# Optimization experiments

Measured on AMD Instinct MI355X. Metric: run time of the kernel, lower is better.

## Reference

```python
import jax, jax.numpy as jnp
import numpy as np
from jax import lax

S, B, C = 128, 32, 16
VW, VC = 100000, 100
DW, DC = 256, 64
HW, HC = 512, 128
T = 17


def setup_inputs():
    key = jax.random.key(0)
    it = iter(jax.random.split(key, 40))

    def p(shape, scale=0.05):
        return jax.random.normal(next(it), shape, jnp.float32) * scale

    inp = {}
    inp['sentence'] = jax.random.randint(next(it), (S, B), 2, VW)
    inp['char'] = jax.random.randint(next(it), (B, S, C), 2, VC)
    inp['tags'] = jax.random.randint(next(it), (S, B), 0, T)
    inp['W_we'] = p((VW, DW)).at[1].set(0.0)  # padding_idx=1 row zeroed
    inp['W_ce'] = p((VC, DC)).at[1].set(0.0)
    Hc2, Hw2 = HC // 2, HW // 2
    for d in ('f', 'b'):
        inp['c_Wih_' + d] = p((4 * Hc2, DC))
        inp['c_Whh_' + d] = p((4 * Hc2, Hc2))
        inp['c_b_' + d] = p((4 * Hc2,))
        inp['w_Wih_' + d] = p((4 * Hw2, DW + HC))
        inp['w_Whh_' + d] = p((4 * Hw2, Hw2))
        inp['w_b_' + d] = p((4 * Hw2,))
    inp['emit_W'] = p((T, HW))
    inp['emit_b'] = p((T,))
    inp['crf_trans'] = p((T, T), 0.1)
    inp['crf_start'] = p((T,), 0.1)
    inp['crf_end'] = p((T,), 0.1)
    return inp


def _lstm(xs, Wih, Whh, b):
    # xs: (L, N, D); torch gate order i,f,g,o
    H = Whh.shape[1]

    def step(carry, x):
        h, c = carry
        g = x @ Wih.T + h @ Whh.T + b
        i, f, gg, o = jnp.split(g, 4, axis=-1)
        c = jax.nn.sigmoid(f) * c + jax.nn.sigmoid(i) * jnp.tanh(gg)
        h = jax.nn.sigmoid(o) * jnp.tanh(c)
        return (h, c), h

    z = jnp.zeros((xs.shape[1], H), xs.dtype)
    (hT, _), hs = lax.scan(step, (z, z), xs)
    return hs, hT


def _bilstm(xs, Wf, Uf, bf, Wb, Ub, bb):
    hs_f, hT_f = _lstm(xs, Wf, Uf, bf)
    hs_b, hT_b = _lstm(xs[::-1], Wb, Ub, bb)
    return jnp.concatenate([hs_f, hs_b[::-1]], axis=-1), hT_f, hT_b


def _crf_nll(em, tags, mask, trans, start, end):
    # em: (S,B,T); pytorch-crf log-likelihood, reduction='sum'; returns -llh
    b_idx = jnp.arange(em.shape[1])
    mf = mask.astype(em.dtype)
    score0 = start[tags[0]] + em[0, b_idx, tags[0]]

    def num_step(carry, inp):
        s, prev = carry
        e_t, t_t, m_t = inp
        s = s + (trans[prev, t_t] + e_t[b_idx, t_t]) * m_t
        prev = jnp.where(m_t > 0, t_t, prev)
        return (s, prev), None

    (num, last), _ = lax.scan(num_step, (score0, tags[0]), (em[1:], tags[1:], mf[1:]))
    num = num + end[last]

    alpha0 = start[None, :] + em[0]

    def den_step(alpha, inp):
        e_t, m_t = inp
        nxt = jax.scipy.special.logsumexp(alpha[:, :, None] + trans[None] + e_t[:, None, :], axis=1)
        return jnp.where(m_t[:, None] > 0, nxt, alpha), None

    alpha, _ = lax.scan(den_step, alpha0, (em[1:], mf[1:]))
    den = jax.scipy.special.logsumexp(alpha + end[None, :], axis=1)
    return -jnp.sum(num - den)


def reference(sentence, char, tags, W_we, W_ce, c_Wih_f, c_Whh_f, c_b_f, c_Wih_b, c_Whh_b, c_b_b, w_Wih_f, w_Whh_f, w_b_f, w_Wih_b, w_Whh_b, w_b_b, emit_W, emit_b, crf_trans, crf_start, crf_end):
    # char features: batch the per-position char BiLSTM across (B*S)
    ce = W_ce[char]  # (B,S,C,DC)
    ce = jnp.transpose(ce, (2, 0, 1, 3)).reshape(C, B * S, DC)
    _, hTf, hTb = _bilstm(ce, c_Wih_f, c_Whh_f, c_b_f, c_Wih_b, c_Whh_b, c_b_b)
    ch = jnp.concatenate([hTf, hTb], axis=-1).reshape(B, S, HC).transpose(1, 0, 2)  # (S,B,HC)
    x = jnp.concatenate([ch, W_we[sentence]], axis=-1)  # (S,B,HC+DW)
    out, _, _ = _bilstm(x, w_Wih_f, w_Whh_f, w_b_f, w_Wih_b, w_Whh_b, w_b_b)  # (S,B,HW)
    em = out @ emit_W.T + emit_b  # (S,B,T)
    mask = sentence != 1
    return _crf_nll(em, tags, mask, crf_trans, crf_start, crf_end)
```

## Files before the change

### kernel.cpp

```cpp
#include <hip/hip_runtime.h>
#include <math.h>

#define SS 128
#define BB 32
#define CC 16
#define DW 256
#define DC 64
#define HC 128
#define KX 384
#define TT 17

typedef __attribute__((ext_vector_type(8))) short bf16x8;
typedef __attribute__((ext_vector_type(4))) float f32x4;
typedef unsigned long long ull_t;

__device__ __forceinline__ float sigf(float x) { return 1.0f / (1.0f + __expf(-x)); }
__device__ __forceinline__ float tanhfast(float x) {
  float xc = fminf(fmaxf(x, -15.f), 15.f);
  float e = __expf(2.f * xc);
  return (e - 1.f) / (e + 1.f);
}
__device__ __forceinline__ unsigned short f2bf(float x) {
  unsigned int u = __float_as_uint(x);
  u += 0x7FFF + ((u >> 16) & 1);
  return (unsigned short)(u >> 16);
}
__device__ __forceinline__ unsigned ld_u32(const unsigned* p) {
  return __hip_atomic_load(p, __ATOMIC_RELAXED, __HIP_MEMORY_SCOPE_AGENT);
}
__device__ __forceinline__ void st_u32(unsigned* p, unsigned v) {
  __hip_atomic_store(p, v, __ATOMIC_RELAXED, __HIP_MEMORY_SCOPE_AGENT);
}
__device__ __forceinline__ ull_t ld_ull(const ull_t* p) {
  return __hip_atomic_load(p, __ATOMIC_RELAXED, __HIP_MEMORY_SCOPE_AGENT);
}
__device__ __forceinline__ void st_ull(ull_t* p, ull_t v) {
  __hip_atomic_store(p, v, __ATOMIC_RELAXED, __HIP_MEMORY_SCOPE_AGENT);
}

__global__ __launch_bounds__(256) void k0_ihvocab(
    const float* __restrict__ Wce,
    const float* __restrict__ WihF, const float* __restrict__ bF,
    const float* __restrict__ WihB, const float* __restrict__ bB,
    float* __restrict__ ihv) {
  int blk = blockIdx.x;
  int d = blk / 100, v = blk % 100;
  const float* Wih = d ? WihB : WihF;
  const float* bb  = d ? bB   : bF;
  __shared__ float ce[DC];
  if (threadIdx.x < DC) ce[threadIdx.x] = Wce[v * DC + threadIdx.x];
  __syncthreads();
  int g = threadIdx.x;
  float acc = bb[g];
  #pragma unroll 16
  for (int k = 0; k < DC; ++k) acc += ce[k] * Wih[g * DC + k];
  ihv[(d * 100 + v) * 256 + g] = acc;
}

__global__ __launch_bounds__(256) void k1_char(
    const int* __restrict__ charidx,
    const float* __restrict__ WhhF, const float* __restrict__ WhhB,
    const float* __restrict__ ihv,
    float* __restrict__ x)
{
  int blk = blockIdx.x;
  int d = blk >> 8;
  int n0 = (blk & 255) * 16;
  const float* Whh = d ? WhhB : WhhF;

  __shared__ float Wl[256 * 64];
  __shared__ float hl[16 * 68];

  for (int i = threadIdx.x; i < 256 * 64; i += 256) {
    int g = i >> 6, k = i & 63;
    Wl[g * 64 + (((k >> 2) ^ (g & 15)) << 2) + (k & 3)] = Whh[i];
  }
  __syncthreads();

  int hh = threadIdx.x & 63;
  int ng = threadIdx.x >> 6;
  float c[4] = {0.f, 0.f, 0.f, 0.f};
  float h[4] = {0.f, 0.f, 0.f, 0.f};
  int bb_[4], ss_[4];
  #pragma unroll
  for (int m = 0; m < 4; ++m) {
    int n = n0 + ng + 4 * m;
    bb_[m] = n >> 7; ss_[m] = n & 127;
  }

  for (int t = 0; t < CC; ++t) {
    int cpos = d ? (CC - 1 - t) : t;
    float acc[4][4];
    #pragma unroll
    for (int m = 0; m < 4; ++m) {
      int v = charidx[bb_[m] * (SS * CC) + ss_[m] * CC + cpos];
      const float* base = ihv + (d * 100 + v) * 256 + hh;
      acc[m][0] = base[0]; acc[m][1] = base[64]; acc[m][2] = base[128]; acc[m][3] = base[192];
    }
    if (t > 0) {
      #pragma unroll 4
      for (int k = 0; k < 64; k += 4) {
        int kc = k >> 2;
        float4 w4[4];
        #pragma unroll
        for (int q = 0; q < 4; ++q)
          w4[q] = *(const float4*)&Wl[(q * 64 + hh) * 64 + ((kc ^ (hh & 15)) << 2)];
        #pragma unroll
        for (int m = 0; m < 4; ++m) {
          float4 h4 = *(const float4*)&hl[(ng + 4 * m) * 68 + k];
          #pragma unroll
          for (int q = 0; q < 4; ++q)
            acc[m][q] += h4.x * w4[q].x + h4.y * w4[q].y + h4.z * w4[q].z + h4.w * w4[q].w;
        }
      }
      __syncthreads();
    }
    #pragma unroll
    for (int m = 0; m < 4; ++m) {
      float ig = sigf(acc[m][0]);
      float fg = sigf(acc[m][1]);
      float gg = tanhfast(acc[m][2]);
      float og = sigf(acc[m][3]);
      c[m] = fg * c[m] + ig * gg;
      h[m] = og * tanhfast(c[m]);
      hl[(ng + 4 * m) * 68 + hh] = h[m];
    }
    __syncthreads();
  }
  #pragma unroll
  for (int m = 0; m < 4; ++m) {
    int row = ss_[m] * BB + bb_[m];
    x[row * KX + d * 64 + hh] = h[m];
  }
}

__global__ __launch_bounds__(64) void k2_we(
    const int* __restrict__ sentence, const float* __restrict__ Wwe,
    float* __restrict__ x) {
  int row = blockIdx.x;
  int idx = sentence[row];
  const float4* src = (const float4*)(Wwe + (size_t)idx * DW);
  float4* dst = (float4*)(x + (size_t)row * KX + HC);
  dst[threadIdx.x] = src[threadIdx.x];
}

__global__ __launch_bounds__(256) void k3_ihgemm(
    const float* __restrict__ x,
    const float* __restrict__ WihF, const float* __restrict__ bF,
    const float* __restrict__ WihB, const float* __restrict__ bB,
    float* __restrict__ wg) {
  int n0 = blockIdx.x * 128;
  int m0 = blockIdx.y * 128;
  int d  = n0 >> 10;
  int gb = n0 & 1023;
  const float* Wih  = d ? WihB : WihF;
  const float* bias = d ? bB   : bF;

  __shared__ float At[32][132];
  __shared__ float Bt[32][132];

  int tid = threadIdx.x;
  int half = tid & 1, r = tid >> 1;
  int tm = tid & 15, tn = tid >> 4;
  float acc[8][8] = {};

  for (int k0 = 0; k0 < KX; k0 += 32) {
    __syncthreads();
    {
      const float4* srcA = (const float4*)(x + (size_t)(m0 + r) * KX + k0 + half * 16);
      const float4* srcB = (const float4*)(Wih + (size_t)(gb + r) * KX + k0 + half * 16);
      #pragma unroll
      for (int q = 0; q < 4; ++q) {
        float4 v = srcA[q];
        int kk = half * 16 + q * 4;
        At[kk + 0][r] = v.x; At[kk + 1][r] = v.y; At[kk + 2][r] = v.z; At[kk + 3][r] = v.w;
      }
      #pragma unroll
      for (int q = 0; q < 4; ++q) {
        float4 v = srcB[q];
        int kk = half * 16 + q * 4;
        Bt[kk + 0][r] = v.x; Bt[kk + 1][r] = v.y; Bt[kk + 2][r] = v.z; Bt[kk + 3][r] = v.w;
      }
    }
    __syncthreads();
    #pragma unroll 8
    for (int k = 0; k < 32; ++k) {
      float4 a0 = *(const float4*)&At[k][tm * 8];
      float4 a1 = *(const float4*)&At[k][tm * 8 + 4];
      float4 b0 = *(const float4*)&Bt[k][tn * 8];
      float4 b1 = *(const float4*)&Bt[k][tn * 8 + 4];
      float av[8] = {a0.x, a0.y, a0.z, a0.w, a1.x, a1.y, a1.z, a1.w};
      float bv[8] = {b0.x, b0.y, b0.z, b0.w, b1.x, b1.y, b1.z, b1.w};
      #pragma unroll
      for (int i = 0; i < 8; ++i)
        #pragma unroll
        for (int jq = 0; jq < 8; ++jq)
          acc[i][jq] += av[i] * bv[jq];
    }
  }
  float bv8[8];
  #pragma unroll
  for (int jq = 0; jq < 8; ++jq) bv8[jq] = bias[gb + tn * 8 + jq];
  #pragma unroll
  for (int i = 0; i < 8; ++i) {
    int m = m0 + tm * 8 + i;
    float* dst = wg + ((size_t)(d * 4096 + m)) * 1024 + gb + tn * 8;
    float4 v0 = {acc[i][0] + bv8[0], acc[i][1] + bv8[1], acc[i][2] + bv8[2], acc[i][3] + bv8[3]};
    float4 v1 = {acc[i][4] + bv8[4], acc[i][5] + bv8[5], acc[i][6] + bv8[6], acc[i][7] + bv8[7]};
    *(float4*)dst = v0; *(float4*)(dst + 4) = v1;
  }
}

__global__ __launch_bounds__(64, 1) void k4_word(
    const float* __restrict__ WhhF, const float* __restrict__ WhhB,
    const float* __restrict__ wg,
    float* __restrict__ outh,
    unsigned short* __restrict__ hbuf,
    unsigned int* __restrict__ flags) {
  const int blk = blockIdx.x;
  const int d = blk >> 4, widx = blk & 15;
  const int l = threadIdx.x;
  const int l15 = l & 15, q4 = l >> 4;
  const int j0w = widx * 16;
  const float* __restrict__ Whh = d ? WhhB : WhhF;
  unsigned short* hb_d = hbuf + d * 16384;
  unsigned int* fl = flags + d * 16;

  __shared__ unsigned short hl[32 * 24];

  bf16x8 Bf[4][8];
  #pragma unroll
  for (int q = 0; q < 4; ++q) {
    const float* wr = Whh + (size_t)(q * 256 + j0w + l15) * 256 + q4 * 8;
    #pragma unroll
    for (int ks = 0; ks < 8; ++ks) {
      float4 lo = *(const float4*)(wr + ks * 32);
      float4 hi = *(const float4*)(wr + ks * 32 + 4);
      bf16x8 f;
      f[0] = (short)f2bf(lo.x); f[1] = (short)f2bf(lo.y);
      f[2] = (short)f2bf(lo.z); f[3] = (short)f2bf(lo.w);
      f[4] = (short)f2bf(hi.x); f[5] = (short)f2bf(hi.y);
      f[6] = (short)f2bf(hi.z); f[7] = (short)f2bf(hi.w);
      Bf[q][ks] = f;
    }
  }

  float cst[8];
  #pragma unroll
  for (int i = 0; i < 8; ++i) cst[i] = 0.f;

  const int rb = l >> 1;
  const int rh = l & 1;

  for (int t = 0; t < SS; ++t) {
    const int s = d ? (SS - 1 - t) : t;

    f32x4 acc[4][2];
    const float* wgs = wg + ((size_t)d * 4096 + (size_t)s * 32) * 1024 + j0w + l15;
    #pragma unroll
    for (int q = 0; q < 4; ++q)
      #pragma unroll
      for (int mt = 0; mt < 2; ++mt)
        #pragma unroll
        for (int r = 0; r < 4; ++r)
          acc[q][mt][r] = wgs[(size_t)(q4 * 4 + r + mt * 16) * 1024 + q * 256];

    if (t > 0) {
      for (;;) {
        unsigned tg = ld_u32(fl + l15);
        if (__all((int)(tg >= (unsigned)t))) break;
        __builtin_amdgcn_s_sleep(1);
      }

      const unsigned short* hp = hb_d + ((t - 1) & 1) * 8192 + q4 * 8;
      bf16x8 Af[2][8];
      #pragma unroll
      for (int mt = 0; mt < 2; ++mt)
        #pragma unroll
        for (int ks = 0; ks < 8; ++ks) {
          const ull_t* p = (const ull_t*)(hp + (size_t)(l15 + mt * 16) * 256 + ks * 32);
          union { ull_t u[2]; bf16x8 v; } cvt;
          cvt.u[0] = ld_ull(p);
          cvt.u[1] = ld_ull(p + 1);
          Af[mt][ks] = cvt.v;
        }
      #pragma unroll
      for (int q = 0; q < 4; ++q)
        #pragma unroll
        for (int mt = 0; mt < 2; ++mt) {
          f32x4 c = acc[q][mt];
          #pragma unroll
          for (int ks = 0; ks < 8; ++ks)
            c = __builtin_amdgcn_mfma_f32_16x16x32_bf16(Af[mt][ks], Bf[q][ks], c, 0, 0, 0);
          acc[q][mt] = c;
        }
    }

    float hv[8];
    #pragma unroll
    for (int mt = 0; mt < 2; ++mt)
      #pragma unroll
      for (int r = 0; r < 4; ++r) {
        int ix = mt * 4 + r;
        float ig = sigf(acc[0][mt][r]);
        float fg = sigf(acc[1][mt][r]);
        float gg = tanhfast(acc[2][mt][r]);
        float og = sigf(acc[3][mt][r]);
        float c2 = fg * cst[ix] + ig * gg;
        cst[ix] = c2;
        hv[ix] = og * tanhfast(c2);
      }

    #pragma unroll
    for (int mt = 0; mt < 2; ++mt)
      #pragma unroll
      for (int r = 0; r < 4; ++r)
        hl[(q4 * 4 + r + mt * 16) * 24 + l15] = f2bf(hv[mt * 4 + r]);
    ull_t plo = *(const ull_t*)&hl[rb * 24 + rh * 8];
    ull_t phi = *(const ull_t*)&hl[rb * 24 + rh * 8 + 4];
    ull_t* dst = (ull_t*)(hb_d + (t & 1) * 8192 + (size_t)rb * 256 + j0w + rh * 8);
    st_ull(dst, plo);
    st_ull(dst + 1, phi);
    asm volatile("s_waitcnt vmcnt(0)" ::: "memory");
    if (l == 0) st_u32(fl + widx, (unsigned)(t + 1));

    float* op = outh + (size_t)(s * 32) * 512 + d * 256 + j0w + l15;
    #pragma unroll
    for (int mt = 0; mt < 2; ++mt)
      #pragma unroll
      for (int r = 0; r < 4; ++r)
        __builtin_nontemporal_store(hv[mt * 4 + r], op + (size_t)(q4 * 4 + r + mt * 16) * 512);
  }
}

__global__ __launch_bounds__(64) void k5_emit(
    const float* __restrict__ outh, const float* __restrict__ eW,
    const float* __restrict__ eb, float* __restrict__ em) {
  int row = blockIdx.x;
  int t = threadIdx.x;
  if (t < TT) {
    const float4* o4 = (const float4*)(outh + (size_t)row * 512);
    const float4* w4 = (const float4*)(eW + (size_t)t * 512);
    float acc = 0.f;
    #pragma unroll 16
    for (int k = 0; k < 128; ++k) {
      float4 a = o4[k], bq = w4[k];
      acc += a.x * bq.x + a.y * bq.y + a.z * bq.z + a.w * bq.w;
    }
    em[row * TT + t] = acc + eb[t];
  }
}

__global__ __launch_bounds__(64) void k6_crf(
    const int* __restrict__ sentence, const int* __restrict__ tags,
    const float* __restrict__ em, const float* __restrict__ trans,
    const float* __restrict__ startv, const float* __restrict__ endv,
    float* __restrict__ outp) {
  int b = blockIdx.x;
  int j = threadIdx.x;
  __shared__ float ash[TT];
  __shared__ float red[TT];
  float tc[TT];
  float alpha = 0.f;
  if (j < TT) {
    #pragma unroll
    for (int i = 0; i < TT; ++i) tc[i] = trans[i * TT + j];
    alpha = startv[j] + em[(0 * BB + b) * TT + j];
  }
  for (int s = 1; s < SS; ++s) {
    if (j < TT) ash[j] = alpha;
    __syncthreads();
    int m = (sentence[s * BB + b] != 1) ? 1 : 0;
    if (j < TT) {
      float mx = -1e30f;
      #pragma unroll
      for (int i = 0; i < TT; ++i) mx = fmaxf(mx, ash[i] + tc[i]);
      float sum = 0.f;
      #pragma unroll
      for (int i = 0; i < TT; ++i) sum += __expf(ash[i] + tc[i] - mx);
      float nxt = mx + __logf(sum) + em[(s * BB + b) * TT + j];
      if (m) alpha = nxt;
    }
    __syncthreads();
  }
  if (j < TT) red[j] = alpha + endv[j];
  __syncthreads();
  if (j == 0) {
    float mx = -1e30f;
    for (int i = 0; i < TT; ++i) mx = fmaxf(mx, red[i]);
    float sum = 0.f;
    for (int i = 0; i < TT; ++i) sum += __expf(red[i] - mx);
    float den = mx + __logf(sum);
    int prev = tags[0 * BB + b];
    float num = startv[prev] + em[(0 * BB + b) * TT + prev];
    for (int s = 1; s < SS; ++s) {
      int tg = tags[s * BB + b];
      if (sentence[s * BB + b] != 1) {
        num += trans[prev * TT + tg] + em[(s * BB + b) * TT + tg];
        prev = tg;
      }
    }
    num += endv[prev];
    atomicAdd(outp, den - num);
  }
}

extern "C" void kernel_launch(void* const* d_in, const int* in_sizes, int n_in,
                              void* d_out, int out_size, void* d_ws, size_t ws_size,
                              hipStream_t stream) {
  (void)in_sizes; (void)n_in; (void)out_size; (void)ws_size;
  const int*   sentence = (const int*)d_in[0];
  const int*   charidx  = (const int*)d_in[1];
  const int*   tags     = (const int*)d_in[2];
  const float* Wwe   = (const float*)d_in[3];
  const float* Wce   = (const float*)d_in[4];
  const float* cWihF = (const float*)d_in[5];
  const float* cWhhF = (const float*)d_in[6];
  const float* cbF   = (const float*)d_in[7];
  const float* wWihF = (const float*)d_in[8];
  const float* wWhhF = (const float*)d_in[9];
  const float* wbF   = (const float*)d_in[10];
  const float* cWihB = (const float*)d_in[11];
  const float* cWhhB = (const float*)d_in[12];
  const float* cbB   = (const float*)d_in[13];
  const float* wWihB = (const float*)d_in[14];
  const float* wWhhB = (const float*)d_in[15];
  const float* wbB   = (const float*)d_in[16];
  const float* eW    = (const float*)d_in[17];
  const float* eb    = (const float*)d_in[18];
  const float* trans = (const float*)d_in[19];
  const float* startv= (const float*)d_in[20];
  const float* endv  = (const float*)d_in[21];

  char* ws = (char*)d_ws;
  unsigned int*   flags = (unsigned int*)(ws + 0);
  float*          ihv   = (float*)(ws + 512);
  float*          x     = (float*)(ws + 205312);
  float*          wg    = (float*)(ws + 6496768);
  unsigned short* hbuf  = (unsigned short*)(ws + 40051200);
  float*          outh  = (float*)(ws + 40116736);
  float*          em    = (float*)(ws + 48505344);

  hipMemsetAsync(flags, 0, 512, stream);
  hipMemsetAsync(d_out, 0, sizeof(float), stream);

  k0_ihvocab<<<200, 256, 0, stream>>>(Wce, cWihF, cbF, cWihB, cbB, ihv);
  k1_char<<<512, 256, 0, stream>>>(charidx, cWhhF, cWhhB, ihv, x);
  k2_we<<<4096, 64, 0, stream>>>(sentence, Wwe, x);
  k3_ihgemm<<<dim3(16, 32), 256, 0, stream>>>(x, wWihF, wbF, wWihB, wbB, wg);
  k4_word<<<32, 64, 0, stream>>>(wWhhF, wWhhB, wg, outh, hbuf, flags);
  k5_emit<<<4096, 64, 0, stream>>>(outh, eW, eb, em);
  k6_crf<<<32, 64, 0, stream>>>(sentence, tags, em, trans, startv, endv, (float*)d_out);
}
```

Measured before the change: 1.017 ms.

## Convert word LSTM input-projection GEMM to bf16 MFMA with pre-conversion kernel

Adds a kernel that converts the concatenated input x and both input weight matrices to bf16 in a scratch region. The fp32 SIMT register-tiled GEMM is replaced with a 16x16x32 bf16 MFMA GEMM that uses padded LDS tiles. This is meant to cut the compute cost of the 4096x2048x384 projection. It adds a conversion pass and an extra launch, and lowers input precision to bf16. The scratch buffers alias the outh region, which is only written later by the recurrent kernel.

Result: faster. 954.9 us (-6.1%).

```diff
diff --git a/kernel.cpp b/kernel.cpp
--- a/kernel.cpp
+++ b/kernel.cpp
@@ -144,70 +144,90 @@
   dst[threadIdx.x] = src[threadIdx.x];
 }
 
-__global__ __launch_bounds__(256) void k3_ihgemm(
+__global__ __launch_bounds__(256) void kcv(
     const float* __restrict__ x,
-    const float* __restrict__ WihF, const float* __restrict__ bF,
-    const float* __restrict__ WihB, const float* __restrict__ bB,
+    const float* __restrict__ WihF, const float* __restrict__ WihB,
+    unsigned short* __restrict__ xb, unsigned short* __restrict__ wb) {
+  int i = blockIdx.x * 256 + threadIdx.x;
+  const float* src; unsigned short* dst; int off;
+  if (i < 196608)      { src = x;    dst = xb;              off = i; }
+  else if (i < 245760) { src = WihF; dst = wb;              off = i - 196608; }
+  else                 { src = WihB; dst = wb + 1024 * 384; off = i - 245760; }
+  float4 a = *(const float4*)(src + (size_t)off * 8);
+  float4 b = *(const float4*)(src + (size_t)off * 8 + 4);
+  bf16x8 o;
+  o[0] = (short)f2bf(a.x); o[1] = (short)f2bf(a.y);
+  o[2] = (short)f2bf(a.z); o[3] = (short)f2bf(a.w);
+  o[4] = (short)f2bf(b.x); o[5] = (short)f2bf(b.y);
+  o[6] = (short)f2bf(b.z); o[7] = (short)f2bf(b.w);
+  *(bf16x8*)(dst + (size_t)off * 8) = o;
+}
+
+__global__ __launch_bounds__(256) void k3m(
+    const unsigned short* __restrict__ xb, const unsigned short* __restrict__ wb,
+    const float* __restrict__ bF, const float* __restrict__ bB,
     float* __restrict__ wg) {
-  int n0 = blockIdx.x * 128;
-  int m0 = blockIdx.y * 128;
-  int d  = n0 >> 10;
-  int gb = n0 & 1023;
-  const float* Wih  = d ? WihB : WihF;
-  const float* bias = d ? bB   : bF;
-
-  __shared__ float At[32][132];
-  __shared__ float Bt[32][132];
-
-  int tid = threadIdx.x;
-  int half = tid & 1, r = tid >> 1;
-  int tm = tid & 15, tn = tid >> 4;
-  float acc[8][8] = {};
-
-  for (int k0 = 0; k0 < KX; k0 += 32) {
+  const int n0 = blockIdx.x * 128;
+  const int m0 = blockIdx.y * 128;
+  const int d  = n0 >> 10;
+  const int gb0 = n0 & 1023;
+  const float* bias = d ? bB : bF;
+
+  __shared__ unsigned short Ab[128 * 40];
+  __shared__ unsigned short Bb[128 * 40];
+
+  const int tid = threadIdx.x;
+  const int l = tid & 63, w = tid >> 6;
+  const int wm = w >> 1, wn = w & 1;
+  const int l15 = l & 15, q4 = l >> 4;
+  const int sr = tid >> 1, shf = tid & 1;
+
+  f32x4 acc[4][4];
+  #pragma unroll
+  for (int mr = 0; mr < 4; ++mr)
+    #pragma unroll
+    for (int nr = 0; nr < 4; ++nr)
+      acc[mr][nr] = (f32x4){0.f, 0.f, 0.f, 0.f};
+
+  for (int kt = 0; kt < 12; ++kt) {
     __syncthreads();
     {
-      const float4* srcA = (const float4*)(x + (size_t)(m0 + r) * KX + k0 + half * 16);
-      const float4* srcB = (const float4*)(Wih + (size_t)(gb + r) * KX + k0 + half * 16);
-      #pragma unroll
-      for (int q = 0; q < 4; ++q) {
-        float4 v = srcA[q];
-        int kk = half * 16 + q * 4;
-        At[kk + 0][r] = v.x; At[kk + 1][r] = v.y; At[kk + 2][r] = v.z; At[kk + 3][r] = v.w;
-      }
-      #pragma unroll
-      for (int q = 0; q < 4; ++q) {
-        float4 v = srcB[q];
-        int kk = half * 16 + q * 4;
-        Bt[kk + 0][r] = v.x; Bt[kk + 1][r] = v.y; Bt[kk + 2][r] = v.z; Bt[kk + 3][r] = v.w;
-      }
+      const bf16x8* sA = (const bf16x8*)(xb + (size_t)(m0 + sr) * KX + kt * 32 + shf * 16);
+      const bf16x8* sB = (const bf16x8*)(wb + (size_t)(n0 + sr) * KX + kt * 32 + shf * 16);
+      bf16x8 a0 = sA[0], a1 = sA[1];
+      bf16x8 b0 = sB[0], b1 = sB[1];
+      *(bf16x8*)&Ab[sr * 40 + shf * 16]     = a0;
+      *(bf16x8*)&Ab[sr * 40 + shf * 16 + 8] = a1;
+      *(bf16x8*)&Bb[sr * 40 + shf * 16]     = b0;
+      *(bf16x8*)&Bb[sr * 40 + shf * 16 + 8] = b1;
     }
     __syncthreads();
-    #pragma unroll 8
-    for (int k = 0; k < 32; ++k) {
-      float4 a0 = *(const float4*)&At[k][tm * 8];
-      float4 a1 = *(const float4*)&At[k][tm * 8 + 4];
-      float4 b0 = *(const float4*)&Bt[k][tn * 8];
-      float4 b1 = *(const float4*)&Bt[k][tn * 8 + 4];
-      float av[8] = {a0.x, a0.y, a0.z, a0.w, a1.x, a1.y, a1.z, a1.w};
-      float bv[8] = {b0.x, b0.y, b0.z, b0.w, b1.x, b1.y, b1.z, b1.w};
-      #pragma unroll
-      for (int i = 0; i < 8; ++i)
-        #pragma unroll
-        for (int jq = 0; jq < 8; ++jq)
-          acc[i][jq] += av[i] * bv[jq];
-    }
-  }
-  float bv8[8];
-  #pragma unroll
-  for (int jq = 0; jq < 8; ++jq) bv8[jq] = bias[gb + tn * 8 + jq];
-  #pragma unroll
-  for (int i = 0; i < 8; ++i) {
-    int m = m0 + tm * 8 + i;
-    float* dst = wg + ((size_t)(d * 4096 + m)) * 1024 + gb + tn * 8;
-    float4 v0 = {acc[i][0] + bv8[0], acc[i][1] + bv8[1], acc[i][2] + bv8[2], acc[i][3] + bv8[3]};
-    float4 v1 = {acc[i][4] + bv8[4], acc[i][5] + bv8[5], acc[i][6] + bv8[6], acc[i][7] + bv8[7]};
-    *(float4*)dst = v0; *(float4*)(dst + 4) = v1;
+    bf16x8 Afr[4], Bfr[4];
+    #pragma unroll
+    for (int mr = 0; mr < 4; ++mr)
+      Afr[mr] = *(const bf16x8*)&Ab[(wm * 64 + mr * 16 + l15) * 40 + q4 * 8];
+    #pragma unroll
+    for (int nr = 0; nr < 4; ++nr)
+      Bfr[nr] = *(const bf16x8*)&Bb[(wn * 64 + nr * 16 + l15) * 40 + q4 * 8];
+    #pragma unroll
+    for (int mr = 0; mr < 4; ++mr)
+      #pragma unroll
+      for (int nr = 0; nr < 4; ++nr)
+        acc[mr][nr] = __builtin_amdgcn_mfma_f32_16x16x32_bf16(Afr[mr], Bfr[nr], acc[mr][nr], 0, 0, 0);
+  }
+
+  #pragma unroll
+  for (int nr = 0; nr < 4; ++nr) {
+    int gcol = gb0 + wn * 64 + nr * 16 + l15;
+    float bv = bias[gcol];
+    #pragma unroll
+    for (int mr = 0; mr < 4; ++mr) {
+      int mrow = m0 + wm * 64 + mr * 16 + q4 * 4;
+      float* dst = wg + ((size_t)(d * 4096 + mrow)) * 1024 + gcol;
+      #pragma unroll
+      for (int r = 0; r < 4; ++r)
+        dst[(size_t)r * 1024] = acc[mr][nr][r] + bv;
+    }
   }
 }
 
@@ -440,6 +460,8 @@
   unsigned short* hbuf  = (unsigned short*)(ws + 40051200);
   float*          outh  = (float*)(ws + 40116736);
   float*          em    = (float*)(ws + 48505344);
+  unsigned short* xb = (unsigned short*)(ws + 40116736);
+  unsigned short* wb = (unsigned short*)(ws + 40116736 + 3145728);
 
   hipMemsetAsync(flags, 0, 512, stream);
   hipMemsetAsync(d_out, 0, sizeof(float), stream);
@@ -447,7 +469,8 @@
   k0_ihvocab<<<200, 256, 0, stream>>>(Wce, cWihF, cbF, cWihB, cbB, ihv);
   k1_char<<<512, 256, 0, stream>>>(charidx, cWhhF, cWhhB, ihv, x);
   k2_we<<<4096, 64, 0, stream>>>(sentence, Wwe, x);
-  k3_ihgemm<<<dim3(16, 32), 256, 0, stream>>>(x, wWihF, wbF, wWihB, wbB, wg);
+  kcv<<<1152, 256, 0, stream>>>(x, wWihF, wWihB, xb, wb);
+  k3m<<<dim3(16, 32), 256, 0, stream>>>(xb, wb, wbF, wbB, wg);
   k4_word<<<32, 64, 0, stream>>>(wWhhF, wWhhB, wg, outh, hbuf, flags);
   k5_emit<<<4096, 64, 0, stream>>>(outh, eW, eb, em);
   k6_crf<<<32, 64, 0, stream>>>(sentence, tags, em, trans, startv, endv, (float*)d_out);
```
